# Performance work log

Measured on AMD Instinct MI355X. Metric: run time of the kernel, lower is better.

## Reference

```python
import jax, jax.numpy as jnp
import numpy as np

D_MODEL = 512
D_STATE = 16
D_CONV = 4
D_INNER = 1024  # expand_factor * d_model
HEADS = 8
D_K = D_MODEL // HEADS
EPS = 1e-5


def layer_norm(x, g, b):
    mu = jnp.mean(x, axis=-1, keepdims=True)
    var = jnp.var(x, axis=-1, keepdims=True)
    return (x - mu) / jnp.sqrt(var + EPS) * g + b


def silu(x):
    return x * jax.nn.sigmoid(x)


def setup_inputs() -> dict:
    key = jax.random.key(0)
    ks = jax.random.split(key, 20)
    s = 0.02

    def n(k, shape):
        return jax.random.normal(k, shape, jnp.float32) * s

    inp = {
        "x": jax.random.normal(ks[0], (8, 1024, D_MODEL), jnp.float32),
        # Mamba params (Linear weights stored as [in, out])
        "in_proj_w": n(ks[1], (D_MODEL, 2 * D_INNER)),
        "conv_w": n(ks[2], (D_INNER, D_CONV)),
        "conv_b": jnp.zeros((D_INNER,), jnp.float32),
        "x_proj_w": n(ks[3], (D_INNER, 2 * D_STATE)),
        "dt_proj_w": n(ks[4], (D_INNER, D_INNER)),
        "dt_proj_b": jnp.zeros((D_INNER,), jnp.float32),
        "A_log": jnp.log(jnp.arange(1, D_STATE + 1, dtype=jnp.float32)),
        "D": jnp.ones((D_INNER,), jnp.float32),
        "out_proj_w": n(ks[5], (D_INNER, D_MODEL)),
        # attention
        "wq_w": n(ks[6], (D_MODEL, D_MODEL)), "wq_b": jnp.zeros((D_MODEL,), jnp.float32),
        "wk_w": n(ks[7], (D_MODEL, D_MODEL)), "wk_b": jnp.zeros((D_MODEL,), jnp.float32),
        "wv_w": n(ks[8], (D_MODEL, D_MODEL)), "wv_b": jnp.zeros((D_MODEL,), jnp.float32),
        "wo_w": n(ks[9], (D_MODEL, D_MODEL)), "wo_b": jnp.zeros((D_MODEL,), jnp.float32),
        "attn_ln_g": jnp.ones((D_MODEL,), jnp.float32), "attn_ln_b": jnp.zeros((D_MODEL,), jnp.float32),
        # FFN
        "ffn_w1": n(ks[10], (D_MODEL, 4 * D_MODEL)), "ffn_b1": jnp.zeros((4 * D_MODEL,), jnp.float32),
        "ffn_w2": n(ks[11], (4 * D_MODEL, D_MODEL)), "ffn_b2": jnp.zeros((D_MODEL,), jnp.float32),
        # norms
        "norm1_g": jnp.ones((D_MODEL,), jnp.float32), "norm1_b": jnp.zeros((D_MODEL,), jnp.float32),
        "norm2_g": jnp.ones((D_MODEL,), jnp.float32), "norm2_b": jnp.zeros((D_MODEL,), jnp.float32),
        "norm3_g": jnp.ones((D_MODEL,), jnp.float32), "norm3_b": jnp.zeros((D_MODEL,), jnp.float32),
        # gate
        "gate_w": n(ks[12], (2 * D_MODEL, D_MODEL)), "gate_b": jnp.zeros((D_MODEL,), jnp.float32),
    }
    return inp


def selective_scan(u, delta, A, B, C, Dp):
    # u, delta: [b, L, d_inner]; B, C: [b, L, d_state]; A: [d_state]; Dp: [d_inner]
    def step(h, inp):
        u_i, d_i, B_i, C_i = inp
        dA = jnp.exp(d_i[:, None, :] * A[None, :, None])        # [b, S, di]
        h = h * dA + (d_i[:, None, :] * B_i[:, :, None]) * u_i[:, None, :]
        y_i = jnp.sum(h * C_i[:, :, None], axis=1)              # [b, di]
        return h, y_i

    b = u.shape[0]
    h0 = jnp.zeros((b, A.shape[0], u.shape[-1]), u.dtype)
    xs = (u.transpose(1, 0, 2), delta.transpose(1, 0, 2),
          B.transpose(1, 0, 2), C.transpose(1, 0, 2))
    _, ys = jax.lax.scan(step, h0, xs)                          # [L, b, di]
    y = ys.transpose(1, 0, 2)
    return y + u * Dp


def mamba(x, in_proj_w, conv_w, conv_b, x_proj_w, dt_proj_w, dt_proj_b, A_log, Dp, out_proj_w):
    L = x.shape[1]
    xr = x @ in_proj_w
    xm, res = jnp.split(xr, 2, axis=-1)                         # [b, L, di] each
    # causal depthwise conv1d: left pad d_conv-1
    xp = jnp.pad(xm, ((0, 0), (D_CONV - 1, 0), (0, 0)))
    xc = sum(conv_w[:, k] * xp[:, k:k + L, :] for k in range(D_CONV)) + conv_b
    xc = silu(xc)
    BC = xc @ x_proj_w
    B, C = jnp.split(BC, 2, axis=-1)                            # [b, L, d_state]
    delta = jax.nn.softplus(xc @ dt_proj_w + dt_proj_b)
    A = -jnp.exp(A_log)
    y = selective_scan(xc, delta, A, B, C, Dp)
    y = y * silu(res)
    return y @ out_proj_w


def attention(q_in, wq_w, wq_b, wk_w, wk_b, wv_w, wv_b, wo_w, wo_b, ln_g, ln_b):
    b, S, _ = q_in.shape
    Q = (q_in @ wq_w + wq_b).reshape(b, S, HEADS, D_K)
    K = (q_in @ wk_w + wk_b).reshape(b, S, HEADS, D_K)
    V = (q_in @ wv_w + wv_b).reshape(b, S, HEADS, D_K)
    scores = jnp.einsum('bqhd,bkhd->bhqk', Q, K) / np.sqrt(D_K).astype(np.float32)
    w = jax.nn.softmax(scores, axis=-1)
    out = jnp.einsum('bhqk,bkhd->bqhd', w, V).reshape(b, S, D_MODEL)
    out = out @ wo_w + wo_b
    return layer_norm(out + q_in, ln_g, ln_b), w


def reference(x, in_proj_w, conv_w, conv_b, x_proj_w, dt_proj_w, dt_proj_b, A_log, D,
              out_proj_w, wq_w, wq_b, wk_w, wk_b, wv_w, wv_b, wo_w, wo_b,
              attn_ln_g, attn_ln_b, ffn_w1, ffn_b1, ffn_w2, ffn_b2,
              norm1_g, norm1_b, norm2_g, norm2_b, norm3_g, norm3_b, gate_w, gate_b):
    mamba_out = mamba(layer_norm(x, norm1_g, norm1_b), in_proj_w, conv_w, conv_b,
                      x_proj_w, dt_proj_w, dt_proj_b, A_log, D, out_proj_w)
    x = x + mamba_out
    xn = layer_norm(x, norm2_g, norm2_b)
    attn_out, attn_w = attention(xn, wq_w, wq_b, wk_w, wk_b, wv_w, wv_b, wo_w, wo_b,
                                 attn_ln_g, attn_ln_b)
    x = x + attn_out
    combined = jnp.concatenate([mamba_out, attn_out], axis=-1)
    g = jax.nn.sigmoid(combined @ gate_w + gate_b)
    fused = g * mamba_out + (1.0 - g) * attn_out
    x = x + fused
    xn3 = layer_norm(x, norm3_g, norm3_b)
    ffn = jax.nn.gelu(xn3 @ ffn_w1 + ffn_b1) @ ffn_w2 + ffn_b2
    x = x + ffn
    return (x, attn_w)
```

## Files before the change

### kernel.cpp

```cpp
#include <hip/hip_runtime.h>

#define SEQL 1024
#define DMODEL 512
#define DINNER 1024
#define NROWS 8192
#define SEG 64
#define NSEG 16
#define LOG2E 1.4426950408889634f

typedef unsigned short u16;
typedef unsigned int u32;
using bf16x8 = __attribute__((ext_vector_type(8))) short;
using f32x4  = __attribute__((ext_vector_type(4))) float;
using u16x4  = __attribute__((ext_vector_type(4))) unsigned short;

__device__ __forceinline__ float rcp_fast(float x){ return __builtin_amdgcn_rcpf(x); }
__device__ __forceinline__ float exp_fast(float x){ return __expf(x); }
#if __has_builtin(__builtin_amdgcn_exp2f)
__device__ __forceinline__ float exp2_fast(float x){ return __builtin_amdgcn_exp2f(x); }
#else
__device__ __forceinline__ float exp2_fast(float x){ return __expf(x*0.6931471805599453f); }
#endif
__device__ __forceinline__ float sigmoid_f(float x){ return rcp_fast(1.f+exp_fast(-x)); }
__device__ __forceinline__ float softplus_f(float x){ return fmaxf(x,0.f)+__logf(1.f+exp_fast(-fabsf(x))); }
__device__ __forceinline__ float gelu_f(float x){
  float u2 = 1.5957691216057308f*(x+0.044715f*x*x*x);
  float t = 1.f - 2.f*rcp_fast(1.f+exp_fast(u2));
  return 0.5f*x*(1.f+t);
}
__device__ __forceinline__ u16 f2bf(float f){
  u32 u = __builtin_bit_cast(u32, f);
  return (u16)((u + 0x7FFFu + ((u>>16)&1u)) >> 16);
}
__device__ __forceinline__ float bf2f(u16 h){
  return __builtin_bit_cast(float, (u32)h << 16);
}

typedef __attribute__((address_space(1))) const void g_void;
typedef __attribute__((address_space(3))) void l_void;
__device__ __forceinline__ void gl_lds16(const void* g, void* l){
  __builtin_amdgcn_global_load_lds((g_void*)g, (l_void*)l, 16, 0, 0);
}

struct WtDesc { const float* src; u16* dst; int K; int N; int t0; };
struct WtArgs { WtDesc d[11]; };

__global__ __launch_bounds__(256) void wt_k(WtArgs a)
{
  __shared__ float t[64][65];
  int bid = blockIdx.x;
  int i = 0;
  #pragma unroll
  for (int j=1;j<11;++j) if (bid >= a.d[j].t0) i = j;
  const float* src = a.d[i].src; u16* dst = a.d[i].dst;
  int K = a.d[i].K, N = a.d[i].N;
  int ntN = (N+63)>>6;
  int loc = bid - a.d[i].t0;
  int k0 = (loc / ntN)*64, n0 = (loc % ntN)*64;
  int tr = threadIdx.x>>4, tc = threadIdx.x&15;
  #pragma unroll
  for (int p=0;p<4;++p) {
    int r = p*16 + tr; int c = tc*4;
    if (n0 + c < N) {
      float4 v = *(const float4*)(src + (size_t)(k0+r)*N + n0 + c);
      t[r][c]=v.x; t[r][c+1]=v.y; t[r][c+2]=v.z; t[r][c+3]=v.w;
    }
  }
  __syncthreads();
  #pragma unroll
  for (int p=0;p<4;++p) {
    int n = p*16 + tr; int k = tc*4;
    if (n0 + n < N) {
      u16x4 o = { f2bf(t[k][n]), f2bf(t[k+1][n]), f2bf(t[k+2][n]), f2bf(t[k+3][n]) };
      *(u16x4*)(dst + (size_t)(n0+n)*K + k0 + k) = o;
    }
  }
}

__global__ __launch_bounds__(256) void pack3_k(const float* a, const float* b,
                                               const float* c, float* o)
{
  int t = blockIdx.x*256 + threadIdx.x;
  if (t < 512) o[t] = a[t];
  else if (t < 1024) o[t] = b[t-512];
  else if (t < 1536) o[t] = c[t-1024];
}

__global__ __launch_bounds__(128) void ln_k(const float* a, const float* b, float* resid,
                                            const float* g, const float* beta,
                                            float* outf, u16* outb)
{
  int row = blockIdx.x;
  int t = threadIdx.x;
  size_t off = (size_t)row*DMODEL + t*4;
  float4 v = *(const float4*)(a + off);
  if (b) {
    float4 w = *(const float4*)(b + off);
    v.x += w.x; v.y += w.y; v.z += w.z; v.w += w.w;
  }
  if (resid) *(float4*)(resid + off) = v;
  float s = v.x+v.y+v.z+v.w;
  float q = v.x*v.x+v.y*v.y+v.z*v.z+v.w*v.w;
  #pragma unroll
  for (int o=1;o<64;o<<=1){ s += __shfl_xor(s,o); q += __shfl_xor(q,o); }
  __shared__ float ss[2], qq[2];
  int w = t>>6;
  if ((t&63)==0){ ss[w]=s; qq[w]=q; }
  __syncthreads();
  s = ss[0]+ss[1]; q = qq[0]+qq[1];
  float mean = s*(1.f/512.f);
  float var  = q*(1.f/512.f) - mean*mean;
  float rstd = rsqrtf(var + 1e-5f);
  int c = t*4;
  float4 gg = *(const float4*)(g+c);
  float4 bb = *(const float4*)(beta+c);
  float4 o4;
  o4.x = (v.x-mean)*rstd*gg.x + bb.x;
  o4.y = (v.y-mean)*rstd*gg.y + bb.y;
  o4.z = (v.z-mean)*rstd*gg.z + bb.z;
  o4.w = (v.w-mean)*rstd*gg.w + bb.w;
  if (outf) *(float4*)(outf + off) = o4;
  if (outb) {
    u16x4 ob = { f2bf(o4.x), f2bf(o4.y), f2bf(o4.z), f2bf(o4.w) };
    *(u16x4*)(outb + off) = ob;
  }
}

template<int EPI, int BMODE, int TN>
__global__ __launch_bounds__(256) void mm_k(
    const u16* Ab, int lda, const u16* Bb, int ldb,
    void* Cv, int ldc, int M, int N, int K,
    const float* bias, const float* p0, const float* p1, const float* p2,
    const u16* A2b, u16* aux)
{
  constexpr int NJ = TN/32;
  __shared__ u16 As[128][32];
  __shared__ u16 Bs[TN][32];
  const int tid = threadIdx.x;
  const int bx = blockIdx.x, by = blockIdx.y;
  float* Cf = (float*)Cv;
  u16* Cb = (u16*)Cv;
  const int row0 = by*128, col0 = bx*TN;
  const int sr = tid>>2, sc = tid&3;
  const int wv = tid>>6, lane = tid&63;
  const int wr = wv>>1, wc = wv&1;
  const int lr = lane&15, lk = (lane>>4)*8;
  const int lq = lane>>4;

  f32x4 acc[4][NJ];
  #pragma unroll
  for (int i=0;i<4;++i)
    #pragma unroll
    for (int j=0;j<NJ;++j)
      acc[i][j] = (f32x4){0.f,0.f,0.f,0.f};

  for (int k0=0; k0<K; k0+=32) {
    #pragma unroll
    for (int h=0; h<2; ++h) {
      int row = sr + h*64;
      const u16* src;
      if (BMODE==3) {
        int kk = k0 + sc*8;
        src = (kk < 512) ? Ab + (size_t)(row0+row)*512 + kk
                         : A2b + (size_t)(row0+row)*512 + (kk-512);
      } else {
        src = Ab + (size_t)(row0+row)*lda + k0 + sc*8;
      }
      gl_lds16(src, &As[row][sc*8]);
    }
    #pragma unroll
    for (int h=0; h<TN/64; ++h) {
      int rowb = sr + h*64;
      gl_lds16(Bb + (size_t)(col0+rowb)*ldb + k0 + sc*8, &Bs[rowb][sc*8]);
    }
    __syncthreads();
    bf16x8 fa[4], fb[NJ];
    #pragma unroll
    for (int i=0;i<4;++i) fa[i] = *(const bf16x8*)&As[wr*64 + i*16 + lr][lk];
    #pragma unroll
    for (int j=0;j<NJ;++j) fb[j] = *(const bf16x8*)&Bs[wc*(TN/2) + j*16 + lr][lk];
    #pragma unroll
    for (int i=0;i<4;++i)
      #pragma unroll
      for (int j=0;j<NJ;++j)
        acc[i][j] = __builtin_amdgcn_mfma_f32_16x16x32_bf16(fa[i], fb[j], acc[i][j], 0,0,0);
    __syncthreads();
  }

  #pragma unroll
  for (int i=0;i<4;++i) {
    #pragma unroll
    for (int j=0;j<NJ;++j) {
      int col = col0 + wc*(TN/2) + j*16 + lr;
      if (col >= N) continue;
      int rowbase = row0 + wr*64 + i*16 + lq*4;
      f32x4 v4 = acc[i][j];
      if (EPI==11 && col >= 1024) {
        int c2 = col-1024;
        int b2 = rowbase >> 10;
        int l2 = rowbase & 1023;
        float bv = bias[col];
        u16x4 pk = { f2bf(v4[0]+bv), f2bf(v4[1]+bv), f2bf(v4[2]+bv), f2bf(v4[3]+bv) };
        *(u16x4*)(aux + (size_t)b2*DMODEL*SEQL + (size_t)c2*SEQL + l2) = pk;
        continue;
      }
      #pragma unroll
      for (int r=0;r<4;++r) {
        int row = rowbase + r;
        size_t idx = (size_t)row*ldc + col;
        float v = v4[r];
        if (EPI==1) Cf[idx] = v + bias[col];
        else if (EPI==3) Cb[idx] = f2bf(gelu_f(v + bias[col]));
        else if (EPI==5) Cf[idx] = v + bias[col] + p0[idx];
        else if (EPI==6) {
          float g = sigmoid_f(v + bias[col]);
          float m = p0[idx], at = p1[idx];
          Cf[idx] = p2[idx] + at + g*m + (1.f-g)*at;
        }
        else if (EPI==7) Cb[idx] = f2bf(v);
        else if (EPI==9) { Cf[idx] = v; aux[idx] = f2bf(v); }
        else if (EPI==11) {
          size_t i2 = (size_t)(col>>9)*4194304 + (size_t)row*512 + (col&511);
          Cb[i2] = f2bf(v + bias[col]);
        }
        else if (EPI==12) {
          if (col < 32) Cf[(size_t)row*32 + col] = v;
          else aux[(size_t)row*1024 + (col-32)] = f2bf(softplus_f(v + bias[col-32]));
        }
      }
    }
  }
}

__global__ __launch_bounds__(256) void attn_k(const u16* Qb, const u16* Kb,
                                              const u16* VTb, float* AW, u16* Hbb)
{
  __shared__ u16 Qs[16][72];
  __shared__ u16 Ps[16][1032];
  __shared__ float part[4][16][64];
  __shared__ float smax[4][16];
  __shared__ float ssum[4][16];

  const int tid = threadIdx.x;
  const int w = tid>>6, lane = tid&63;
  const int qt = blockIdx.x, bh = blockIdx.y;
  const int b = bh>>3, h = bh&7;
  const int q0 = qt*16;
  const int lr = lane&15, lg = lane>>4;

  {
    int r = tid>>4, c = (tid&15)*4;
    const u16* src = Qb + ((size_t)(b*1024 + q0 + r))*512 + h*64 + c;
    *(u16x4*)&Qs[r][c] = *(const u16x4*)src;
  }
  __syncthreads();

  f32x4 acc[16];
  #pragma unroll
  for (int j=0;j<16;++j) acc[j] = (f32x4){0.f,0.f,0.f,0.f};
  bf16x8 fa0 = *(const bf16x8*)&Qs[lr][lg*8];
  bf16x8 fa1 = *(const bf16x8*)&Qs[lr][32+lg*8];
  const u16* Kbase = Kb + ((size_t)(b*1024 + w*256))*512 + h*64;
  #pragma unroll
  for (int j=0;j<16;++j){
    const u16* krow = Kbase + (size_t)(j*16 + lr)*512 + lg*8;
    bf16x8 fb0 = *(const bf16x8*)krow;
    bf16x8 fb1 = *(const bf16x8*)(krow+32);
    acc[j] = __builtin_amdgcn_mfma_f32_16x16x32_bf16(fa0, fb0, acc[j], 0,0,0);
    acc[j] = __builtin_amdgcn_mfma_f32_16x16x32_bf16(fa1, fb1, acc[j], 0,0,0);
  }

  const int rw = lg*4;
  float m0=-1e30f,m1=-1e30f,m2=-1e30f,m3=-1e30f;
  #pragma unroll
  for (int j=0;j<16;++j){
    m0=fmaxf(m0,acc[j][0]); m1=fmaxf(m1,acc[j][1]);
    m2=fmaxf(m2,acc[j][2]); m3=fmaxf(m3,acc[j][3]);
  }
  #pragma unroll
  for (int o=1;o<16;o<<=1){
    m0=fmaxf(m0,__shfl_xor(m0,o)); m1=fmaxf(m1,__shfl_xor(m1,o));
    m2=fmaxf(m2,__shfl_xor(m2,o)); m3=fmaxf(m3,__shfl_xor(m3,o));
  }
  if (lr==0){ smax[w][rw]=m0; smax[w][rw+1]=m1; smax[w][rw+2]=m2; smax[w][rw+3]=m3; }
  __syncthreads();
  float M0 = fmaxf(fmaxf(smax[0][rw  ],smax[1][rw  ]),fmaxf(smax[2][rw  ],smax[3][rw  ]));
  float M1 = fmaxf(fmaxf(smax[0][rw+1],smax[1][rw+1]),fmaxf(smax[2][rw+1],smax[3][rw+1]));
  float M2 = fmaxf(fmaxf(smax[0][rw+2],smax[1][rw+2]),fmaxf(smax[2][rw+2],smax[3][rw+2]));
  float M3 = fmaxf(fmaxf(smax[0][rw+3],smax[1][rw+3]),fmaxf(smax[2][rw+3],smax[3][rw+3]));
  const float cs = 0.125f*LOG2E;
  float s0=0.f,s1=0.f,s2=0.f,s3=0.f;
  #pragma unroll
  for (int j=0;j<16;++j){
    acc[j][0]=exp2_fast((acc[j][0]-M0)*cs); s0+=acc[j][0];
    acc[j][1]=exp2_fast((acc[j][1]-M1)*cs); s1+=acc[j][1];
    acc[j][2]=exp2_fast((acc[j][2]-M2)*cs); s2+=acc[j][2];
    acc[j][3]=exp2_fast((acc[j][3]-M3)*cs); s3+=acc[j][3];
  }
  #pragma unroll
  for (int o=1;o<16;o<<=1){
    s0+=__shfl_xor(s0,o); s1+=__shfl_xor(s1,o);
    s2+=__shfl_xor(s2,o); s3+=__shfl_xor(s3,o);
  }
  if (lr==0){ ssum[w][rw]=s0; ssum[w][rw+1]=s1; ssum[w][rw+2]=s2; ssum[w][rw+3]=s3; }
  __syncthreads();
  float i0 = rcp_fast(ssum[0][rw  ]+ssum[1][rw  ]+ssum[2][rw  ]+ssum[3][rw  ]);
  float i1 = rcp_fast(ssum[0][rw+1]+ssum[1][rw+1]+ssum[2][rw+1]+ssum[3][rw+1]);
  float i2 = rcp_fast(ssum[0][rw+2]+ssum[1][rw+2]+ssum[2][rw+2]+ssum[3][rw+2]);
  float i3 = rcp_fast(ssum[0][rw+3]+ssum[1][rw+3]+ssum[2][rw+3]+ssum[3][rw+3]);

  float* awr = AW + (size_t)bh*1048576 + (size_t)q0*1024 + (size_t)w*256;
  #pragma unroll
  for (int j=0;j<16;++j){
    int col = j*16 + lr;
    float v0=acc[j][0]*i0, v1=acc[j][1]*i1, v2=acc[j][2]*i2, v3=acc[j][3]*i3;
    awr[(size_t)(rw  )*1024 + col] = v0;
    awr[(size_t)(rw+1)*1024 + col] = v1;
    awr[(size_t)(rw+2)*1024 + col] = v2;
    awr[(size_t)(rw+3)*1024 + col] = v3;
    Ps[rw  ][w*256+col] = f2bf(v0);
    Ps[rw+1][w*256+col] = f2bf(v1);
    Ps[rw+2][w*256+col] = f2bf(v2);
    Ps[rw+3][w*256+col] = f2bf(v3);
  }
  __syncthreads();

  f32x4 av[4];
  #pragma unroll
  for (int j2=0;j2<4;++j2) av[j2] = (f32x4){0.f,0.f,0.f,0.f};
  const u16* Vbase = VTb + (size_t)b*524288 + (size_t)(h*64)*1024 + w*256;
  #pragma unroll
  for (int ks=0; ks<8; ++ks){
    bf16x8 pa = *(const bf16x8*)&Ps[lr][w*256 + ks*32 + lg*8];
    #pragma unroll
    for (int j2=0;j2<4;++j2){
      bf16x8 fb = *(const bf16x8*)(Vbase + (size_t)(j2*16+lr)*1024 + ks*32 + lg*8);
      av[j2] = __builtin_amdgcn_mfma_f32_16x16x32_bf16(pa, fb, av[j2], 0,0,0);
    }
  }
  #pragma unroll
  for (int j2=0;j2<4;++j2){
    part[w][rw  ][j2*16+lr] = av[j2][0];
    part[w][rw+1][j2*16+lr] = av[j2][1];
    part[w][rw+2][j2*16+lr] = av[j2][2];
    part[w][rw+3][j2*16+lr] = av[j2][3];
  }
  __syncthreads();
  {
    int q = tid>>4, dd = (tid&15)*4;
    float4 o0 = *(float4*)&part[0][q][dd];
    float4 o1 = *(float4*)&part[1][q][dd];
    float4 o2 = *(float4*)&part[2][q][dd];
    float4 o3 = *(float4*)&part[3][q][dd];
    float ox = o0.x+o1.x+o2.x+o3.x;
    float oy = o0.y+o1.y+o2.y+o3.y;
    float oz = o0.z+o1.z+o2.z+o3.z;
    float ow = o0.w+o1.w+o2.w+o3.w;
    u16x4 ob = { f2bf(ox), f2bf(oy), f2bf(oz), f2bf(ow) };
    *(u16x4*)(Hbb + ((size_t)(b*1024+q0+q))*512 + h*64 + dd) = ob;
  }
}

__global__ __launch_bounds__(256) void conv_k(const u16* xrb, const float* cw,
                                              const float* cb, u16* xcb)
{
  int t = blockIdx.x*256 + threadIdx.x;
  int d = (t & 255)*4;
  int row = t >> 8;
  int l = row & (SEQL-1);
  const u16* xmb = xrb + (size_t)(row - l)*2048 + d;
  float wv[4][4];
  #pragma unroll
  for (int dd=0; dd<4; ++dd){
    float4 w = *(const float4*)(cw + (size_t)(d+dd)*4);
    wv[dd][0]=w.x; wv[dd][1]=w.y; wv[dd][2]=w.z; wv[dd][3]=w.w;
  }
  float4 acc = *(const float4*)(cb + d);
  #pragma unroll
  for (int k=0;k<4;++k){
    int ls = l + k - 3;
    if (ls >= 0) {
      u16x4 xv = *(const u16x4*)(xmb + (size_t)ls*2048);
      acc.x += wv[0][k]*bf2f(xv[0]);
      acc.y += wv[1][k]*bf2f(xv[1]);
      acc.z += wv[2][k]*bf2f(xv[2]);
      acc.w += wv[3][k]*bf2f(xv[3]);
    }
  }
  float sx = acc.x*rcp_fast(1.f+exp_fast(-acc.x));
  float sy = acc.y*rcp_fast(1.f+exp_fast(-acc.y));
  float sz = acc.z*rcp_fast(1.f+exp_fast(-acc.z));
  float sw = acc.w*rcp_fast(1.f+exp_fast(-acc.w));
  size_t off = (size_t)row*DINNER + d;
  u16x4 ob = { f2bf(sx), f2bf(sy), f2bf(sz), f2bf(sw) };
  *(u16x4*)(xcb + off) = ob;
}

__global__ __launch_bounds__(256) void scan1_k(const u16* dtb, const u16* ub,
                                               const float* bc, const float* A_log,
                                               float* Pq)
{
  const int tid = threadIdx.x;
  const int d   = blockIdx.x*256 + tid;
  const int seg = blockIdx.y;
  const int b   = blockIdx.z;
  const int l0  = seg*SEG;

  __shared__ float BCs[SEG*32];
  {
    const float4* src = (const float4*)(bc + ((size_t)b*SEQL + l0)*32);
    float4* dst = (float4*)BCs;
    dst[tid]     = src[tid];
    dst[tid+256] = src[tid+256];
  }
  float As2[16];
  #pragma unroll
  for (int s=0;s<16;++s) As2[s] = -expf(A_log[s]) * LOG2E;
  __syncthreads();

  float h[16], P[16];
  #pragma unroll
  for (int s=0;s<16;++s){ h[s]=0.f; P[s]=1.f; }

  size_t base = ((size_t)b*SEQL + l0)*DINNER + d;
  const u16* pdt = dtb + base;
  const u16* pu  = ub  + base;

  u16 dpf[8], upf[8];
  #pragma unroll
  for (int j=0;j<8;++j){ dpf[j]=pdt[(size_t)j*DINNER]; upf[j]=pu[(size_t)j*DINNER]; }
  const u16* pdt_f = pdt + (size_t)8*DINNER;
  const u16* pu_f  = pu  + (size_t)8*DINNER;

  for (int l=0; l<SEG; l+=8) {
    bool pf = (l+8 < SEG);
    #pragma unroll
    for (int j=0;j<8;++j) {
      float dt = bf2f(dpf[j]), u = bf2f(upf[j]);
      if (pf) { dpf[j] = *pdt_f; upf[j] = *pu_f; }
      pdt_f += DINNER; pu_f += DINNER;
      float dtu = dt*u;
      const float* Bs = &BCs[(l+j)*32];
      #pragma unroll
      for (int s=0;s<16;++s) {
        float dA = exp2_fast(dt*As2[s]);
        P[s] *= dA;
        h[s] = fmaf(h[s], dA, dtu*Bs[s]);
      }
    }
  }
  float* out = Pq + (((size_t)b*NSEG + seg)*32)*1024 + d;
  #pragma unroll
  for (int s=0;s<16;++s) {
    out[(size_t)s*1024]      = P[s];
    out[(size_t)(16+s)*1024] = h[s];
  }
}

__global__ __launch_bounds__(256) void scan2_k(const u16* dtb, const u16* ub,
                                               const float* bc, const u16* xrb,
                                               const float* A_log, const float* Dp,
                                               const float* Pq, u16* yb)
{
  const int tid = threadIdx.x;
  const int d   = blockIdx.x*256 + tid;
  const int seg = blockIdx.y;
  const int b   = blockIdx.z;
  const int l0  = seg*SEG;

  __shared__ float BCs[SEG*32];
  {
    const float4* src = (const float4*)(bc + ((size_t)b*SEQL + l0)*32);
    float4* dst = (float4*)BCs;
    dst[tid]     = src[tid];
    dst[tid+256] = src[tid+256];
  }
  float As2[16];
  #pragma unroll
  for (int s=0;s<16;++s) As2[s] = -expf(A_log[s]) * LOG2E;
  float dcoef = Dp[d];
  __syncthreads();

  float h[16];
  #pragma unroll
  for (int s=0;s<16;++s) h[s]=0.f;

  const float* pp = Pq + ((size_t)b*NSEG)*32*1024 + d;
  for (int sg=0; sg<seg; ++sg) {
    const float* q = pp + (size_t)sg*32*1024;
    #pragma unroll
    for (int s=0;s<16;++s)
      h[s] = fmaf(h[s], q[(size_t)s*1024], q[(size_t)(16+s)*1024]);
  }

  size_t rbase = (size_t)b*SEQL + l0;
  const u16* pdt = dtb + rbase*DINNER + d;
  const u16* pu  = ub  + rbase*DINNER + d;
  const u16* pr  = xrb + rbase*2048 + 1024 + d;
  u16*       py  = yb  + rbase*DINNER + d;

  u16 dpf[8], upf[8], rpf[8];
  #pragma unroll
  for (int j=0;j<8;++j){
    dpf[j]=pdt[(size_t)j*DINNER]; upf[j]=pu[(size_t)j*DINNER]; rpf[j]=pr[(size_t)j*2048];
  }
  const u16* pdt_f = pdt + (size_t)8*DINNER;
  const u16* pu_f  = pu  + (size_t)8*DINNER;
  const u16* pr_f  = pr  + (size_t)8*2048;

  for (int l=0; l<SEG; l+=8) {
    bool pf = (l+8 < SEG);
    #pragma unroll
    for (int j=0;j<8;++j) {
      float dt = bf2f(dpf[j]), u = bf2f(upf[j]), rv = bf2f(rpf[j]);
      if (pf) { dpf[j] = *pdt_f; upf[j] = *pu_f; rpf[j] = *pr_f; }
      pdt_f += DINNER; pu_f += DINNER; pr_f += 2048;
      float dtu = dt*u;
      float acc = 0.f;
      const float* Bs = &BCs[(l+j)*32];
      #pragma unroll
      for (int s=0;s<16;++s) {
        float dA = exp2_fast(dt*As2[s]);
        h[s] = fmaf(h[s], dA, dtu*Bs[s]);
        acc  = fmaf(h[s], Bs[16+s], acc);
      }
      float y = fmaf(u, dcoef, acc);
      y *= rv * rcp_fast(1.f + exp2_fast(rv*(-LOG2E)));
      *py = f2bf(y);
      py += DINNER;
    }
  }
}

extern "C" void kernel_launch(void* const* d_in, const int* in_sizes, int n_in,
                              void* d_out, int out_size, void* d_ws, size_t ws_size,
                              hipStream_t stream)
{
  const float* x          = (const float*)d_in[0];
  const float* in_proj_w  = (const float*)d_in[1];
  const float* conv_w     = (const float*)d_in[2];
  const float* conv_b     = (const float*)d_in[3];
  const float* x_proj_w   = (const float*)d_in[4];
  const float* dt_proj_w  = (const float*)d_in[5];
  const float* dt_proj_b  = (const float*)d_in[6];
  const float* A_log      = (const float*)d_in[7];
  const float* Dvec       = (const float*)d_in[8];
  const float* out_proj_w = (const float*)d_in[9];
  const float* wq_w = (const float*)d_in[10]; const float* wq_b = (const float*)d_in[11];
  const float* wk_w = (const float*)d_in[12]; const float* wk_b = (const float*)d_in[13];
  const float* wv_w = (const float*)d_in[14]; const float* wv_b = (const float*)d_in[15];
  const float* wo_w = (const float*)d_in[16]; const float* wo_b = (const float*)d_in[17];
  const float* attn_ln_g = (const float*)d_in[18]; const float* attn_ln_b = (const float*)d_in[19];
  const float* ffn_w1 = (const float*)d_in[20]; const float* ffn_b1 = (const float*)d_in[21];
  const float* ffn_w2 = (const float*)d_in[22]; const float* ffn_b2 = (const float*)d_in[23];
  const float* norm1_g = (const float*)d_in[24]; const float* norm1_b = (const float*)d_in[25];
  const float* norm2_g = (const float*)d_in[26]; const float* norm2_b = (const float*)d_in[27];
  const float* norm3_g = (const float*)d_in[28]; const float* norm3_b = (const float*)d_in[29];
  const float* gate_w  = (const float*)d_in[30]; const float* gate_b  = (const float*)d_in[31];

  float* ws  = (float*)d_ws;
  float* BC   = ws;
  float* X1   = BC  + 262144;
  float* XN2  = X1  + 4194304;
  float* MB   = XN2 + 4194304;
  float* WOUT = MB  + 4194304;
  float* ATT  = WOUT+ 4194304;
  float* Pq   = ATT + 4194304;
  u16* WT0 = (u16*)(Pq + 4194304);
  u16* XRb = WT0 + 6324224;
  u16* NB  = XRb + 16777216;
  u16* XCb = NB  + 4194304;
  u16* DTb = XCb + 8388608;
  u16* Yb  = DTb + 8388608;
  float* QKVB = (float*)(Yb + 8388608);

  u16* Qb   = XRb;
  u16* Kb   = XRb + 4194304;
  u16* VTb  = XRb + 8388608;
  u16* Hbb  = XRb + 12582912;
  u16* FHb  = XRb;
  u16* MBb  = XCb;
  u16* ATTb = XCb + 4194304;

  u16* inprojT = WT0;
  u16* xprojT  = inprojT + 1048576;
  u16* dtT     = xprojT  + 32768;
  u16* outT    = dtT     + 1048576;
  u16* wqT     = outT    + 524288;
  u16* wkT     = wqT     + 262144;
  u16* wvT     = wkT     + 262144;
  u16* woT     = wvT     + 262144;
  u16* ffn1T   = woT     + 262144;
  u16* ffn2T   = ffn1T   + 1048576;
  u16* gateT   = ffn2T   + 1048576;

  float* XOUT = (float*)d_out;
  float* AW   = (float*)d_out + 4194304;

  const float* nulf = nullptr;
  u16* nulh = nullptr;

  WtArgs wa;
  wa.d[0]  = { in_proj_w, inprojT, 512, 2048, 0 };
  wa.d[1]  = { x_proj_w,  xprojT, 1024,   32, 256 };
  wa.d[2]  = { dt_proj_w, dtT,    1024, 1024, 272 };
  wa.d[3]  = { out_proj_w,outT,   1024,  512, 528 };
  wa.d[4]  = { wq_w,      wqT,     512,  512, 656 };
  wa.d[5]  = { wk_w,      wkT,     512,  512, 720 };
  wa.d[6]  = { wv_w,      wvT,     512,  512, 784 };
  wa.d[7]  = { wo_w,      woT,     512,  512, 848 };
  wa.d[8]  = { ffn_w1,    ffn1T,   512, 2048, 912 };
  wa.d[9]  = { ffn_w2,    ffn2T,  2048,  512, 1168 };
  wa.d[10] = { gate_w,    gateT,  1024,  512, 1424 };
  wt_k<<<1552, 256, 0, stream>>>(wa);
  pack3_k<<<6, 256, 0, stream>>>(wq_b, wk_b, wv_b, QKVB);

  ln_k<<<NROWS, 128, 0, stream>>>(x, nullptr, nullptr, norm1_g, norm1_b, nullptr, NB);
  mm_k<7,0,128><<<dim3(16,64), 256, 0, stream>>>(NB,512, inprojT,512, XRb,2048,
        NROWS,2048,512, nulf,nulf,nulf,nulf,nulh,nulh);
  conv_k<<<NROWS, 256, 0, stream>>>(XRb, conv_w, conv_b, XCb);
  mm_k<12,0,128><<<dim3(9,64), 256, 0, stream>>>(XCb,1024, xprojT,1024, BC,32,
        NROWS,1056,1024, dt_proj_b,nulf,nulf,nulf,nulh,DTb);
  scan1_k<<<dim3(4,NSEG-1,8), 256, 0, stream>>>(DTb, XCb, BC, A_log, Pq);
  scan2_k<<<dim3(4,NSEG,8),   256, 0, stream>>>(DTb, XCb, BC, XRb, A_log, Dvec, Pq, Yb);
  mm_k<9,0,64><<<dim3(8,64), 256, 0, stream>>>(Yb,1024, outT,1024, MB,512,
        NROWS,512,1024, nulf,nulf,nulf,nulf,nulh,MBb);
  ln_k<<<NROWS, 128, 0, stream>>>(x, MB, X1, norm2_g, norm2_b, XN2, NB);
  mm_k<11,0,128><<<dim3(12,64), 256, 0, stream>>>(NB,512, wqT,512, Qb,512,
        NROWS,1536,512, QKVB,nulf,nulf,nulf,nulh,VTb);
  attn_k<<<dim3(64,64), 256, 0, stream>>>(Qb, Kb, VTb, AW, Hbb);
  mm_k<1,0,64><<<dim3(8,64), 256, 0, stream>>>(Hbb,512, woT,512, WOUT,512,
        NROWS,512,512, wo_b,nulf,nulf,nulf,nulh,nulh);
  ln_k<<<NROWS, 128, 0, stream>>>(WOUT, XN2, nullptr, attn_ln_g, attn_ln_b, ATT, ATTb);
  mm_k<6,3,64><<<dim3(8,64), 256, 0, stream>>>(MBb,512, gateT,1024, X1,512,
        NROWS,512,1024, gate_b, MB, ATT, X1, ATTb, nulh);
  ln_k<<<NROWS, 128, 0, stream>>>(X1, nullptr, nullptr, norm3_g, norm3_b, nullptr, NB);
  mm_k<3,0,128><<<dim3(16,64), 256, 0, stream>>>(NB,512, ffn1T,512, FHb,2048,
        NROWS,2048,512, ffn_b1,nulf,nulf,nulf,nulh,nulh);
  mm_k<5,0,64><<<dim3(8,64), 256, 0, stream>>>(FHb,2048, ffn2T,2048, XOUT,512,
        NROWS,512,2048, ffn_b2, X1,nulf,nulf,nulh,nulh);
}
```

Measured before the change: 628.5 us.

## Keep intermediates in bf16 and process 32 queries per attention block

Several fp32 intermediates (mamba output, attention out-projection, attention layernorm output) are replaced with bf16 buffers, and the layernorm and gate epilogue read them as bf16. This removes fp32 write and read traffic. Attention now handles 32 query rows per block instead of 16, so each K/V load is reused twice. The PV stage splits head dimensions across waves instead of splitting keys, which removes the partial-sum reduction through shared memory. The cost is lower precision in the residual and gate inputs, plus more registers and LDS per attention block.

```diff
diff --git a/kernel.cpp b/kernel.cpp
--- a/kernel.cpp
+++ b/kernel.cpp
@@ -86,17 +86,27 @@
   else if (t < 1536) o[t] = c[t-1024];
 }
 
-__global__ __launch_bounds__(128) void ln_k(const float* a, const float* b, float* resid,
+template<int AM>
+__global__ __launch_bounds__(128) void ln_k(const void* av, const void* bv, float* resid,
                                             const float* g, const float* beta,
                                             float* outf, u16* outb)
 {
   int row = blockIdx.x;
   int t = threadIdx.x;
   size_t off = (size_t)row*DMODEL + t*4;
-  float4 v = *(const float4*)(a + off);
-  if (b) {
-    float4 w = *(const float4*)(b + off);
-    v.x += w.x; v.y += w.y; v.z += w.z; v.w += w.w;
+  float4 v;
+  if (AM==2) {
+    u16x4 va = *(const u16x4*)((const u16*)av + off);
+    v.x = bf2f(va[0]); v.y = bf2f(va[1]); v.z = bf2f(va[2]); v.w = bf2f(va[3]);
+  } else {
+    v = *(const float4*)((const float*)av + off);
+  }
+  if (AM==1) {
+    u16x4 wb = *(const u16x4*)((const u16*)bv + off);
+    v.x += bf2f(wb[0]); v.y += bf2f(wb[1]); v.z += bf2f(wb[2]); v.w += bf2f(wb[3]);
+  } else if (AM==2) {
+    float4 wb = *(const float4*)((const float*)bv + off);
+    v.x += wb.x; v.y += wb.y; v.z += wb.z; v.w += wb.w;
   }
   if (resid) *(float4*)(resid + off) = v;
   float s = v.x+v.y+v.z+v.w;
@@ -209,16 +219,16 @@
         int row = rowbase + r;
         size_t idx = (size_t)row*ldc + col;
         float v = v4[r];
-        if (EPI==1) Cf[idx] = v + bias[col];
-        else if (EPI==3) Cb[idx] = f2bf(gelu_f(v + bias[col]));
+        if (EPI==3) Cb[idx] = f2bf(gelu_f(v + bias[col]));
         else if (EPI==5) Cf[idx] = v + bias[col] + p0[idx];
         else if (EPI==6) {
           float g = sigmoid_f(v + bias[col]);
-          float m = p0[idx], at = p1[idx];
+          float m  = bf2f(((const u16*)p0)[idx]);
+          float at = bf2f(((const u16*)p1)[idx]);
           Cf[idx] = p2[idx] + at + g*m + (1.f-g)*at;
         }
         else if (EPI==7) Cb[idx] = f2bf(v);
-        else if (EPI==9) { Cf[idx] = v; aux[idx] = f2bf(v); }
+        else if (EPI==8) Cb[idx] = f2bf(v + bias[col]);
         else if (EPI==11) {
           size_t i2 = (size_t)(col>>9)*4194304 + (size_t)row*512 + (col&511);
           Cb[i2] = f2bf(v + bias[col]);
@@ -235,129 +245,131 @@
 __global__ __launch_bounds__(256) void attn_k(const u16* Qb, const u16* Kb,
                                               const u16* VTb, float* AW, u16* Hbb)
 {
-  __shared__ u16 Qs[16][72];
-  __shared__ u16 Ps[16][1032];
-  __shared__ float part[4][16][64];
-  __shared__ float smax[4][16];
-  __shared__ float ssum[4][16];
+  __shared__ u16 Qs[32][72];
+  __shared__ u16 Ps[32][1032];
+  __shared__ float smax[4][32];
+  __shared__ float ssum[4][32];
 
   const int tid = threadIdx.x;
   const int w = tid>>6, lane = tid&63;
   const int qt = blockIdx.x, bh = blockIdx.y;
   const int b = bh>>3, h = bh&7;
-  const int q0 = qt*16;
+  const int q0 = qt*32;
   const int lr = lane&15, lg = lane>>4;
+  const int rw = lg*4;
 
   {
-    int r = tid>>4, c = (tid&15)*4;
+    int r = tid>>3, c = (tid&7)*8;
     const u16* src = Qb + ((size_t)(b*1024 + q0 + r))*512 + h*64 + c;
-    *(u16x4*)&Qs[r][c] = *(const u16x4*)src;
-  }
-  __syncthreads();
-
-  f32x4 acc[16];
-  #pragma unroll
-  for (int j=0;j<16;++j) acc[j] = (f32x4){0.f,0.f,0.f,0.f};
-  bf16x8 fa0 = *(const bf16x8*)&Qs[lr][lg*8];
-  bf16x8 fa1 = *(const bf16x8*)&Qs[lr][32+lg*8];
+    *(uint4*)&Qs[r][c] = *(const uint4*)src;
+  }
+  __syncthreads();
+
+  f32x4 acc0[16], acc1[16];
+  #pragma unroll
+  for (int j=0;j<16;++j){ acc0[j]=(f32x4){0.f,0.f,0.f,0.f}; acc1[j]=(f32x4){0.f,0.f,0.f,0.f}; }
+  bf16x8 fa00 = *(const bf16x8*)&Qs[lr][lg*8];
+  bf16x8 fa01 = *(const bf16x8*)&Qs[lr][32+lg*8];
+  bf16x8 fa10 = *(const bf16x8*)&Qs[16+lr][lg*8];
+  bf16x8 fa11 = *(const bf16x8*)&Qs[16+lr][32+lg*8];
   const u16* Kbase = Kb + ((size_t)(b*1024 + w*256))*512 + h*64;
   #pragma unroll
   for (int j=0;j<16;++j){
     const u16* krow = Kbase + (size_t)(j*16 + lr)*512 + lg*8;
     bf16x8 fb0 = *(const bf16x8*)krow;
     bf16x8 fb1 = *(const bf16x8*)(krow+32);
-    acc[j] = __builtin_amdgcn_mfma_f32_16x16x32_bf16(fa0, fb0, acc[j], 0,0,0);
-    acc[j] = __builtin_amdgcn_mfma_f32_16x16x32_bf16(fa1, fb1, acc[j], 0,0,0);
-  }
-
-  const int rw = lg*4;
-  float m0=-1e30f,m1=-1e30f,m2=-1e30f,m3=-1e30f;
-  #pragma unroll
-  for (int j=0;j<16;++j){
-    m0=fmaxf(m0,acc[j][0]); m1=fmaxf(m1,acc[j][1]);
-    m2=fmaxf(m2,acc[j][2]); m3=fmaxf(m3,acc[j][3]);
-  }
-  #pragma unroll
-  for (int o=1;o<16;o<<=1){
-    m0=fmaxf(m0,__shfl_xor(m0,o)); m1=fmaxf(m1,__shfl_xor(m1,o));
-    m2=fmaxf(m2,__shfl_xor(m2,o)); m3=fmaxf(m3,__shfl_xor(m3,o));
-  }
-  if (lr==0){ smax[w][rw]=m0; smax[w][rw+1]=m1; smax[w][rw+2]=m2; smax[w][rw+3]=m3; }
-  __syncthreads();
-  float M0 = fmaxf(fmaxf(smax[0][rw  ],smax[1][rw  ]),fmaxf(smax[2][rw  ],smax[3][rw  ]));
-  float M1 = fmaxf(fmaxf(smax[0][rw+1],smax[1][rw+1]),fmaxf(smax[2][rw+1],smax[3][rw+1]));
-  float M2 = fmaxf(fmaxf(smax[0][rw+2],smax[1][rw+2]),fmaxf(smax[2][rw+2],smax[3][rw+2]));
-  float M3 = fmaxf(fmaxf(smax[0][rw+3],smax[1][rw+3]),fmaxf(smax[2][rw+3],smax[3][rw+3]));
+    acc0[j] = __builtin_amdgcn_mfma_f32_16x16x32_bf16(fa00, fb0, acc0[j], 0,0,0);
+    acc0[j] = __builtin_amdgcn_mfma_f32_16x16x32_bf16(fa01, fb1, acc0[j], 0,0,0);
+    acc1[j] = __builtin_amdgcn_mfma_f32_16x16x32_bf16(fa10, fb0, acc1[j], 0,0,0);
+    acc1[j] = __builtin_amdgcn_mfma_f32_16x16x32_bf16(fa11, fb1, acc1[j], 0,0,0);
+  }
+
+  float mg0[4] = {-1e30f,-1e30f,-1e30f,-1e30f};
+  float mg1[4] = {-1e30f,-1e30f,-1e30f,-1e30f};
+  #pragma unroll
+  for (int j=0;j<16;++j)
+    #pragma unroll
+    for (int r=0;r<4;++r){
+      mg0[r]=fmaxf(mg0[r],acc0[j][r]);
+      mg1[r]=fmaxf(mg1[r],acc1[j][r]);
+    }
+  #pragma unroll
+  for (int o=1;o<16;o<<=1)
+    #pragma unroll
+    for (int r=0;r<4;++r){
+      mg0[r]=fmaxf(mg0[r],__shfl_xor(mg0[r],o));
+      mg1[r]=fmaxf(mg1[r],__shfl_xor(mg1[r],o));
+    }
+  if (lr==0){
+    #pragma unroll
+    for (int r=0;r<4;++r){ smax[w][rw+r]=mg0[r]; smax[w][16+rw+r]=mg1[r]; }
+  }
+  __syncthreads();
+  #pragma unroll
+  for (int r=0;r<4;++r){
+    mg0[r] = fmaxf(fmaxf(smax[0][rw+r],smax[1][rw+r]),fmaxf(smax[2][rw+r],smax[3][rw+r]));
+    mg1[r] = fmaxf(fmaxf(smax[0][16+rw+r],smax[1][16+rw+r]),fmaxf(smax[2][16+rw+r],smax[3][16+rw+r]));
+  }
   const float cs = 0.125f*LOG2E;
-  float s0=0.f,s1=0.f,s2=0.f,s3=0.f;
-  #pragma unroll
-  for (int j=0;j<16;++j){
-    acc[j][0]=exp2_fast((acc[j][0]-M0)*cs); s0+=acc[j][0];
-    acc[j][1]=exp2_fast((acc[j][1]-M1)*cs); s1+=acc[j][1];
-    acc[j][2]=exp2_fast((acc[j][2]-M2)*cs); s2+=acc[j][2];
-    acc[j][3]=exp2_fast((acc[j][3]-M3)*cs); s3+=acc[j][3];
-  }
-  #pragma unroll
-  for (int o=1;o<16;o<<=1){
-    s0+=__shfl_xor(s0,o); s1+=__shfl_xor(s1,o);
-    s2+=__shfl_xor(s2,o); s3+=__shfl_xor(s3,o);
-  }
-  if (lr==0){ ssum[w][rw]=s0; ssum[w][rw+1]=s1; ssum[w][rw+2]=s2; ssum[w][rw+3]=s3; }
-  __syncthreads();
-  float i0 = rcp_fast(ssum[0][rw  ]+ssum[1][rw  ]+ssum[2][rw  ]+ssum[3][rw  ]);
-  float i1 = rcp_fast(ssum[0][rw+1]+ssum[1][rw+1]+ssum[2][rw+1]+ssum[3][rw+1]);
-  float i2 = rcp_fast(ssum[0][rw+2]+ssum[1][rw+2]+ssum[2][rw+2]+ssum[3][rw+2]);
-  float i3 = rcp_fast(ssum[0][rw+3]+ssum[1][rw+3]+ssum[2][rw+3]+ssum[3][rw+3]);
+  float sg0[4]={0.f,0.f,0.f,0.f}, sg1[4]={0.f,0.f,0.f,0.f};
+  #pragma unroll
+  for (int j=0;j<16;++j)
+    #pragma unroll
+    for (int r=0;r<4;++r){
+      acc0[j][r]=exp2_fast((acc0[j][r]-mg0[r])*cs); sg0[r]+=acc0[j][r];
+      acc1[j][r]=exp2_fast((acc1[j][r]-mg1[r])*cs); sg1[r]+=acc1[j][r];
+    }
+  #pragma unroll
+  for (int o=1;o<16;o<<=1)
+    #pragma unroll
+    for (int r=0;r<4;++r){
+      sg0[r]+=__shfl_xor(sg0[r],o);
+      sg1[r]+=__shfl_xor(sg1[r],o);
+    }
+  if (lr==0){
+    #pragma unroll
+    for (int r=0;r<4;++r){ ssum[w][rw+r]=sg0[r]; ssum[w][16+rw+r]=sg1[r]; }
+  }
+  __syncthreads();
+  float ig0[4], ig1[4];
+  #pragma unroll
+  for (int r=0;r<4;++r){
+    ig0[r] = rcp_fast(ssum[0][rw+r]+ssum[1][rw+r]+ssum[2][rw+r]+ssum[3][rw+r]);
+    ig1[r] = rcp_fast(ssum[0][16+rw+r]+ssum[1][16+rw+r]+ssum[2][16+rw+r]+ssum[3][16+rw+r]);
+  }
 
   float* awr = AW + (size_t)bh*1048576 + (size_t)q0*1024 + (size_t)w*256;
   #pragma unroll
   for (int j=0;j<16;++j){
     int col = j*16 + lr;
-    float v0=acc[j][0]*i0, v1=acc[j][1]*i1, v2=acc[j][2]*i2, v3=acc[j][3]*i3;
-    awr[(size_t)(rw  )*1024 + col] = v0;
-    awr[(size_t)(rw+1)*1024 + col] = v1;
-    awr[(size_t)(rw+2)*1024 + col] = v2;
-    awr[(size_t)(rw+3)*1024 + col] = v3;
-    Ps[rw  ][w*256+col] = f2bf(v0);
-    Ps[rw+1][w*256+col] = f2bf(v1);
-    Ps[rw+2][w*256+col] = f2bf(v2);
-    Ps[rw+3][w*256+col] = f2bf(v3);
-  }
-  __syncthreads();
-
-  f32x4 av[4];
-  #pragma unroll
-  for (int j2=0;j2<4;++j2) av[j2] = (f32x4){0.f,0.f,0.f,0.f};
-  const u16* Vbase = VTb + (size_t)b*524288 + (size_t)(h*64)*1024 + w*256;
-  #pragma unroll
-  for (int ks=0; ks<8; ++ks){
-    bf16x8 pa = *(const bf16x8*)&Ps[lr][w*256 + ks*32 + lg*8];
-    #pragma unroll
-    for (int j2=0;j2<4;++j2){
-      bf16x8 fb = *(const bf16x8*)(Vbase + (size_t)(j2*16+lr)*1024 + ks*32 + lg*8);
-      av[j2] = __builtin_amdgcn_mfma_f32_16x16x32_bf16(pa, fb, av[j2], 0,0,0);
-    }
-  }
-  #pragma unroll
-  for (int j2=0;j2<4;++j2){
-    part[w][rw  ][j2*16+lr] = av[j2][0];
-    part[w][rw+1][j2*16+lr] = av[j2][1];
-    part[w][rw+2][j2*16+lr] = av[j2][2];
-    part[w][rw+3][j2*16+lr] = av[j2][3];
-  }
-  __syncthreads();
-  {
-    int q = tid>>4, dd = (tid&15)*4;
-    float4 o0 = *(float4*)&part[0][q][dd];
-    float4 o1 = *(float4*)&part[1][q][dd];
-    float4 o2 = *(float4*)&part[2][q][dd];
-    float4 o3 = *(float4*)&part[3][q][dd];
-    float ox = o0.x+o1.x+o2.x+o3.x;
-    float oy = o0.y+o1.y+o2.y+o3.y;
-    float oz = o0.z+o1.z+o2.z+o3.z;
-    float ow = o0.w+o1.w+o2.w+o3.w;
-    u16x4 ob = { f2bf(ox), f2bf(oy), f2bf(oz), f2bf(ow) };
-    *(u16x4*)(Hbb + ((size_t)(b*1024+q0+q))*512 + h*64 + dd) = ob;
+    #pragma unroll
+    for (int r=0;r<4;++r){
+      float v0 = acc0[j][r]*ig0[r];
+      float v1 = acc1[j][r]*ig1[r];
+      awr[(size_t)(rw+r)*1024 + col] = v0;
+      awr[(size_t)(16+rw+r)*1024 + col] = v1;
+      Ps[rw+r][w*256+col] = f2bf(v0);
+      Ps[16+rw+r][w*256+col] = f2bf(v1);
+    }
+  }
+  __syncthreads();
+
+  f32x4 av0 = (f32x4){0.f,0.f,0.f,0.f};
+  f32x4 av1 = (f32x4){0.f,0.f,0.f,0.f};
+  const u16* Vbase = VTb + (size_t)b*524288 + (size_t)(h*64 + w*16 + lr)*1024;
+  #pragma unroll
+  for (int ks=0; ks<32; ++ks){
+    bf16x8 fb  = *(const bf16x8*)(Vbase + ks*32 + lg*8);
+    bf16x8 pa0 = *(const bf16x8*)&Ps[lr][ks*32 + lg*8];
+    bf16x8 pa1 = *(const bf16x8*)&Ps[16+lr][ks*32 + lg*8];
+    av0 = __builtin_amdgcn_mfma_f32_16x16x32_bf16(pa0, fb, av0, 0,0,0);
+    av1 = __builtin_amdgcn_mfma_f32_16x16x32_bf16(pa1, fb, av1, 0,0,0);
+  }
+  u16* ob = Hbb + ((size_t)(b*1024 + q0))*512 + h*64 + w*16 + lr;
+  #pragma unroll
+  for (int r=0;r<4;++r){
+    ob[(size_t)(rw+r)*512]    = f2bf(av0[r]);
+    ob[(size_t)(16+rw+r)*512] = f2bf(av1[r]);
   }
 }
 
@@ -562,10 +574,7 @@
   float* BC   = ws;
   float* X1   = BC  + 262144;
   float* XN2  = X1  + 4194304;
-  float* MB   = XN2 + 4194304;
-  float* WOUT = MB  + 4194304;
-  float* ATT  = WOUT+ 4194304;
-  float* Pq   = ATT + 4194304;
+  float* Pq   = XN2 + 4194304;
   u16* WT0 = (u16*)(Pq + 4194304);
   u16* XRb = WT0 + 6324224;
   u16* NB  = XRb + 16777216;
@@ -581,6 +590,7 @@
   u16* FHb  = XRb;
   u16* MBb  = XCb;
   u16* ATTb = XCb + 4194304;
+  u16* WOUTb= DTb;
 
   u16* inprojT = WT0;
   u16* xprojT  = inprojT + 1048576;
@@ -615,7 +625,7 @@
   wt_k<<<1552, 256, 0, stream>>>(wa);
   pack3_k<<<6, 256, 0, stream>>>(wq_b, wk_b, wv_b, QKVB);
 
-  ln_k<<<NROWS, 128, 0, stream>>>(x, nullptr, nullptr, norm1_g, norm1_b, nullptr, NB);
+  ln_k<0><<<NROWS, 128, 0, stream>>>(x, nullptr, nullptr, norm1_g, norm1_b, nullptr, NB);
   mm_k<7,0,128><<<dim3(16,64), 256, 0, stream>>>(NB,512, inprojT,512, XRb,2048,
         NROWS,2048,512, nulf,nulf,nulf,nulf,nulh,nulh);
   conv_k<<<NROWS, 256, 0, stream>>>(XRb, conv_w, conv_b, XCb);
@@ -623,18 +633,18 @@
         NROWS,1056,1024, dt_proj_b,nulf,nulf,nulf,nulh,DTb);
   scan1_k<<<dim3(4,NSEG-1,8), 256, 0, stream>>>(DTb, XCb, BC, A_log, Pq);
   scan2_k<<<dim3(4,NSEG,8),   256, 0, stream>>>(DTb, XCb, BC, XRb, A_log, Dvec, Pq, Yb);
-  mm_k<9,0,64><<<dim3(8,64), 256, 0, stream>>>(Yb,1024, outT,1024, MB,512,
-        NROWS,512,1024, nulf,nulf,nulf,nulf,nulh,MBb);
-  ln_k<<<NROWS, 128, 0, stream>>>(x, MB, X1, norm2_g, norm2_b, XN2, NB);
+  mm_k<7,0,64><<<dim3(8,64), 256, 0, stream>>>(Yb,1024, outT,1024, MBb,512,
+        NROWS,512,1024, nulf,nulf,nulf,nulf,nulh,nulh);
+  ln_k<1><<<NROWS, 128, 0, stream>>>(x, MBb, X1, norm2_g, norm2_b, XN2, NB);
   mm_k<11,0,128><<<dim3(12,64), 256, 0, stream>>>(NB,512, wqT,512, Qb,512,
         NROWS,1536,512, QKVB,nulf,nulf,nulf,nulh,VTb);
-  attn_k<<<dim3(64,64), 256, 0, stream>>>(Qb, Kb, VTb, AW, Hbb);
-  mm_k<1,0,64><<<dim3(8,64), 256, 0, stream>>>(Hbb,512, woT,512, WOUT,512,
+  attn_k<<<dim3(32,64), 256, 0, stream>>>(Qb, Kb, VTb, AW, Hbb);
+  mm_k<8,0,64><<<dim3(8,64), 256, 0, stream>>>(Hbb,512, woT,512, WOUTb,512,
         NROWS,512,512, wo_b,nulf,nulf,nulf,nulh,nulh);
-  ln_k<<<NROWS, 128, 0, stream>>>(WOUT, XN2, nullptr, attn_ln_g, attn_ln_b, ATT, ATTb);
+  ln_k<2><<<NROWS, 128, 0, stream>>>(WOUTb, XN2, nullptr, attn_ln_g, attn_ln_b, nullptr, ATTb);
   mm_k<6,3,64><<<dim3(8,64), 256, 0, stream>>>(MBb,512, gateT,1024, X1,512,
-        NROWS,512,1024, gate_b, MB, ATT, X1, ATTb, nulh);
-  ln_k<<<NROWS, 128, 0, stream>>>(X1, nullptr, nullptr, norm3_g, norm3_b, nullptr, NB);
+        NROWS,512,1024, gate_b, (const float*)MBb, (const float*)ATTb, X1, ATTb, nulh);
+  ln_k<0><<<NROWS, 128, 0, stream>>>(X1, nullptr, nullptr, norm3_g, norm3_b, nullptr, NB);
   mm_k<3,0,128><<<dim3(16,64), 256, 0, stream>>>(NB,512, ffn1T,512, FHb,2048,
         NROWS,2048,512, ffn_b1,nulf,nulf,nulf,nulh,nulh);
   mm_k<5,0,64><<<dim3(8,64), 256, 0, stream>>>(FHb,2048, ffn2T,2048, XOUT,512,
```

Measured after the change: 613.7 us. -2.4%, faster.
